# Performance work log

Hardware: AMD Instinct MI355X
Metric: run time of the kernel (lower is better)

The kernel has to match this reference:

```python
import jax, jax.numpy as jnp
import numpy as np

N_HEAD = 16
HEAD_DIM = 64
R_VALUE = 256
EPS_LN = 1e-5


def _orf(x, omega, b):
    # orthogonal random features: sqrt(2/r) * cos(x @ omega.T + b)
    r = b.shape[0]
    return jnp.sqrt(2.0 / r) * jnp.cos(x @ omega.T + b)


def _layernorm(x, gamma, beta):
    m = jnp.mean(x, axis=-1, keepdims=True)
    v = jnp.var(x, axis=-1, keepdims=True)
    return (x - m) / jnp.sqrt(v + EPS_LN) * gamma + beta


def setup_inputs() -> dict:
    key = jax.random.key(0)
    ks = jax.random.split(key, 12)
    B, L = 4, 2048
    dm = N_HEAD * HEAD_DIM  # 1024
    inp = {}
    inp["pre_query"] = jax.random.normal(ks[0], (B, L, dm), jnp.float32)
    inp["pre_key"] = jax.random.normal(ks[1], (B, L, dm), jnp.float32)
    inp["pre_value"] = jax.random.normal(ks[2], (B, L, dm), jnp.float32)
    inp["wq"] = jax.random.normal(ks[3], (dm, dm), jnp.float32) * 0.02
    inp["wk"] = jax.random.normal(ks[4], (dm, dm), jnp.float32) * 0.02
    inp["wv"] = jax.random.normal(ks[5], (dm, dm), jnp.float32) * 0.02
    inp["wo"] = jax.random.normal(ks[6], (dm, dm), jnp.float32) * 0.02
    inp["gamma"] = jnp.ones((dm,), jnp.float32)
    inp["beta"] = jnp.zeros((dm,), jnp.float32)
    G = jax.random.normal(ks[7], (R_VALUE, HEAD_DIM), jnp.float32)
    omega, _ = jnp.linalg.qr(G)  # (r, head_dim), orthonormal columns
    inp["omega"] = omega
    inp["b"] = jax.random.uniform(ks[8], (R_VALUE,), jnp.float32) * 2.0 * jnp.pi
    return inp


def reference(pre_query, pre_key, pre_value, wq, wk, wv, wo, gamma, beta, omega, b):
    B, L, dm = pre_query.shape
    H, D = N_HEAD, dm // N_HEAD
    q = (pre_query @ wq.T).reshape(B, L, H, D)
    k = (pre_key @ wk.T).reshape(B, L, H, D)
    v = (pre_value @ wv.T).reshape(B, L, H, D)

    qp = _orf(q, omega, b)  # (B,L,H,R)
    kp = _orf(k, omega, b)  # (B,L,H,R)

    # causal Performer attention as a linear-attention recurrence:
    # S_t = S_{t-1} + k'_t v_t^T ; z_t = z_{t-1} + k'_t
    # out_t = (q'_t . S_t) / clamp(q'_t . z_t)
    R = b.shape[0]
    S0 = jnp.zeros((B, H, R, D), qp.dtype)
    z0 = jnp.zeros((B, H, R), qp.dtype)

    def step(carry, xs):
        S, z = carry
        q_t, k_t, v_t = xs  # (B,H,R),(B,H,R),(B,H,D)
        S = S + k_t[..., :, None] * v_t[..., None, :]
        z = z + k_t
        num = jnp.einsum('bhr,bhrd->bhd', q_t, S)
        den = jnp.clip(jnp.einsum('bhr,bhr->bh', q_t, z), 1e-6, None)
        return (S, z), num / (den[..., None] + 1e-6)

    xs = (qp.transpose(1, 0, 2, 3), kp.transpose(1, 0, 2, 3), v.transpose(1, 0, 2, 3))
    _, out = jax.lax.scan(step, (S0, z0), xs)  # (L,B,H,D)
    out = out.transpose(1, 0, 2, 3).reshape(B, L, dm)

    pre_result = out @ wo.T
    return _layernorm(pre_result + pre_query, gamma, beta)
```

## Files before the change

### kernel.cpp

```cpp
#include <hip/hip_runtime.h>
#include <hip/hip_bf16.h>


typedef float f4 __attribute__((ext_vector_type(4)));
typedef __attribute__((ext_vector_type(8))) short bf16x8;
typedef __attribute__((ext_vector_type(4))) float f32x4;
typedef unsigned short u16x4 __attribute__((ext_vector_type(4)));
typedef unsigned short u16x8 __attribute__((ext_vector_type(8)));

#define B_  4
#define L_  2048
#define H_  16
#define D_  64
#define DM_ 1024
#define R_  256
#define C_  64
#define NC_ (L_ / C_)
#define M_  (B_ * L_)
#define M2_ (M_ * H_)

static __device__ __forceinline__ unsigned short f2bu(float x) {
    __hip_bfloat16 h = __float2bfloat16(x);
    return *(unsigned short*)&h;
}
static __device__ __forceinline__ float bu2f(unsigned short u) {
    union { unsigned int i; float f; } c; c.i = ((unsigned int)u) << 16; return c.f;
}

typedef __attribute__((address_space(3))) void lds_void_t;
typedef __attribute__((address_space(1))) const void gvoid_t;
static __device__ __forceinline__ void gload16(const void* g, void* l) {
    __builtin_amdgcn_global_load_lds((gvoid_t*)g, (lds_void_t*)l, 16, 0, 0);
}

__launch_bounds__(256)
__global__ void cvt_bf16(const float* __restrict__ in, unsigned short* __restrict__ out, int n4) {
    int i = blockIdx.x * 256 + threadIdx.x;
    if (i < n4) {
        f4 v = *(const f4*)&in[(size_t)i * 4];
        ushort4 o;
        o.x = f2bu(v[0]); o.y = f2bu(v[1]); o.z = f2bu(v[2]); o.w = f2bu(v[3]);
        *(ushort4*)&out[(size_t)i * 4] = o;
    }
}

__launch_bounds__(256)
__global__ void cvt_bf16_x3(const float* __restrict__ i0, const float* __restrict__ i1,
                            const float* __restrict__ i2,
                            unsigned short* __restrict__ o0, unsigned short* __restrict__ o1,
                            unsigned short* __restrict__ o2, int n4) {
    const int z = blockIdx.z;
    const float* in = (z == 0) ? i0 : (z == 1) ? i1 : i2;
    unsigned short* out = (z == 0) ? o0 : (z == 1) ? o1 : o2;
    int i = blockIdx.x * 256 + threadIdx.x;
    if (i < n4) {
        f4 v = *(const f4*)&in[(size_t)i * 4];
        ushort4 o;
        o.x = f2bu(v[0]); o.y = f2bu(v[1]); o.z = f2bu(v[2]); o.w = f2bu(v[3]);
        *(ushort4*)&out[(size_t)i * 4] = o;
    }
}

__launch_bounds__(256)
__global__ void cvt_bf16_x4(const float* __restrict__ i0, const float* __restrict__ i1,
                            const float* __restrict__ i2, const float* __restrict__ i3,
                            unsigned short* __restrict__ o0, unsigned short* __restrict__ o1,
                            unsigned short* __restrict__ o2, unsigned short* __restrict__ o3,
                            int n4_abc, int n4_d) {
    const int z = blockIdx.z;
    const float* in = (z == 0) ? i0 : (z == 1) ? i1 : (z == 2) ? i2 : i3;
    unsigned short* out = (z == 0) ? o0 : (z == 1) ? o1 : (z == 2) ? o2 : o3;
    const int n4 = (z == 3) ? n4_d : n4_abc;
    int i = blockIdx.x * 256 + threadIdx.x;
    if (i < n4) {
        f4 v = *(const f4*)&in[(size_t)i * 4];
        ushort4 o;
        o.x = f2bu(v[0]); o.y = f2bu(v[1]); o.z = f2bu(v[2]); o.w = f2bu(v[3]);
        *(ushort4*)&out[(size_t)i * 4] = o;
    }
}

__launch_bounds__(256)
__global__ void gemm_mfma_b3(const unsigned short* __restrict__ A0, const unsigned short* __restrict__ A1,
                             const unsigned short* __restrict__ A2,
                             const unsigned short* __restrict__ B0, const unsigned short* __restrict__ B1,
                             const unsigned short* __restrict__ B2,
                             unsigned short* __restrict__ C0, unsigned short* __restrict__ C1,
                             unsigned short* __restrict__ C2,
                             int M, int N, int K) {
    __shared__ unsigned short Asl[3][128 * 32];
    __shared__ unsigned short Bsl[3][128 * 32];
    const int z = blockIdx.z;
    const unsigned short* A  = (z == 0) ? A0 : (z == 1) ? A1 : A2;
    const unsigned short* Bw = (z == 0) ? B0 : (z == 1) ? B1 : B2;
    unsigned short*       Cb = (z == 0) ? C0 : (z == 1) ? C1 : C2;
    const int t = threadIdx.x;
    const int lane = t & 63, w = t >> 6;
    const int wr = w >> 1, wc = w & 1;
    const int nwg = gridDim.x * gridDim.y;
    const int bid = blockIdx.y * gridDim.x + blockIdx.x;
    const int cpx = nwg >> 3;
    const int swz = (bid & 7) * cpx + (bid >> 3);
    const int row0 = (swz / gridDim.x) * 128, col0 = (swz % gridDim.x) * 128;
    const int sr0 = t >> 2;
    const int ssw = (((t & 3) ^ ((t >> 3) & 3)) * 8);
    const int lg = lane >> 4, lr = lane & 15;
    const int aslot = (lg ^ ((lr >> 1) & 3)) * 8;

#define STAGE_B3(buf, kkk) do { \
        gload16(&A [(size_t)(row0 + sr0)      * K + (kkk) + ssw], &Asl[buf][t * 8]); \
        gload16(&A [(size_t)(row0 + sr0 + 64) * K + (kkk) + ssw], &Asl[buf][(t + 256) * 8]); \
        gload16(&Bw[(size_t)(col0 + sr0)      * K + (kkk) + ssw], &Bsl[buf][t * 8]); \
        gload16(&Bw[(size_t)(col0 + sr0 + 64) * K + (kkk) + ssw], &Bsl[buf][(t + 256) * 8]); \
    } while (0)
#define COMPUTE_B3(buf) do { \
        bf16x8 af[4], bfr[4]; \
        _Pragma("unroll") \
        for (int m = 0; m < 4; ++m) \
            af[m] = *(const bf16x8*)&Asl[buf][(wr * 64 + m * 16 + lr) * 32 + aslot]; \
        _Pragma("unroll") \
        for (int n = 0; n < 4; ++n) \
            bfr[n] = *(const bf16x8*)&Bsl[buf][(wc * 64 + n * 16 + lr) * 32 + aslot]; \
        _Pragma("unroll") \
        for (int m = 0; m < 4; ++m) \
            _Pragma("unroll") \
            for (int n = 0; n < 4; ++n) \
                acc[m][n] = __builtin_amdgcn_mfma_f32_16x16x32_bf16(af[m], bfr[n], acc[m][n], 0, 0, 0); \
    } while (0)

    f32x4 acc[4][4] = {};
    STAGE_B3(0, 0);
    STAGE_B3(1, 32);
    int cur = 0;
    for (int kk = 0; kk + 64 < K; kk += 32) {
        int nx = cur + 2; if (nx >= 3) nx -= 3;
        STAGE_B3(nx, kk + 64);
        asm volatile("s_waitcnt vmcnt(8)" ::: "memory");
        __builtin_amdgcn_sched_barrier(0);
        __builtin_amdgcn_s_barrier();
        COMPUTE_B3(cur);
        __builtin_amdgcn_s_barrier();
        cur = (cur == 2) ? 0 : cur + 1;
    }
    asm volatile("s_waitcnt vmcnt(4)" ::: "memory");
    __builtin_amdgcn_sched_barrier(0);
    __builtin_amdgcn_s_barrier();
    COMPUTE_B3(cur);
    __builtin_amdgcn_s_barrier();
    cur = (cur == 2) ? 0 : cur + 1;
    asm volatile("s_waitcnt vmcnt(0)" ::: "memory");
    __builtin_amdgcn_sched_barrier(0);
    __builtin_amdgcn_s_barrier();
    COMPUTE_B3(cur);
#undef STAGE_B3
#undef COMPUTE_B3
#pragma unroll
    for (int m = 0; m < 4; ++m)
#pragma unroll
        for (int n = 0; n < 4; ++n)
#pragma unroll
            for (int i = 0; i < 4; ++i) {
                int r  = row0 + wr * 64 + m * 16 + lg * 4 + i;
                int cc = col0 + wc * 64 + n * 16 + lr;
                Cb[(size_t)r * N + cc] = f2bu(acc[m][n][i]);
            }
}

__launch_bounds__(256)
__global__ void gemm_out(const unsigned short* __restrict__ A,
                         const unsigned short* __restrict__ Bw,
                         const float* __restrict__ resid,
                         float* __restrict__ Cf,
                         int M, int N, int K) {
    __shared__ unsigned short Asl[3][64 * 32];
    __shared__ unsigned short Bsl[3][128 * 32];
    const int t = threadIdx.x;
    const int lane = t & 63, w = t >> 6;
    const int nwg = gridDim.x * gridDim.y;
    const int bid = blockIdx.y * gridDim.x + blockIdx.x;
    const int cpx = nwg >> 3;
    const int swz = (bid & 7) * cpx + (bid >> 3);
    const int row0 = (swz / gridDim.x) * 64, col0 = (swz % gridDim.x) * 128;
    const int sr0 = t >> 2;
    const int ssw = (((t & 3) ^ ((t >> 3) & 3)) * 8);
    const int lg = lane >> 4, lr = lane & 15;
    const int aslot = (lg ^ ((lr >> 1) & 3)) * 8;

#define STAGE_O(buf, kkk) do { \
        gload16(&A [(size_t)(row0 + sr0)      * K + (kkk) + ssw], &Asl[buf][t * 8]); \
        gload16(&Bw[(size_t)(col0 + sr0)      * K + (kkk) + ssw], &Bsl[buf][t * 8]); \
        gload16(&Bw[(size_t)(col0 + sr0 + 64) * K + (kkk) + ssw], &Bsl[buf][(t + 256) * 8]); \
    } while (0)
#define COMPUTE_O(buf) do { \
        bf16x8 af[4], bfr[2]; \
        _Pragma("unroll") \
        for (int m = 0; m < 4; ++m) \
            af[m] = *(const bf16x8*)&Asl[buf][(m * 16 + lr) * 32 + aslot]; \
        _Pragma("unroll") \
        for (int n = 0; n < 2; ++n) \
            bfr[n] = *(const bf16x8*)&Bsl[buf][(w * 32 + n * 16 + lr) * 32 + aslot]; \
        _Pragma("unroll") \
        for (int m = 0; m < 4; ++m) \
            _Pragma("unroll") \
            for (int n = 0; n < 2; ++n) \
                acc[m][n] = __builtin_amdgcn_mfma_f32_16x16x32_bf16(af[m], bfr[n], acc[m][n], 0, 0, 0); \
    } while (0)

    f32x4 acc[4][2] = {};
    STAGE_O(0, 0);
    STAGE_O(1, 32);
    int cur = 0;
    for (int kk = 0; kk + 64 < K; kk += 32) {
        int nx = cur + 2; if (nx >= 3) nx -= 3;
        STAGE_O(nx, kk + 64);
        asm volatile("s_waitcnt vmcnt(6)" ::: "memory");
        __builtin_amdgcn_sched_barrier(0);
        __builtin_amdgcn_s_barrier();
        COMPUTE_O(cur);
        __builtin_amdgcn_s_barrier();
        cur = (cur == 2) ? 0 : cur + 1;
    }
    asm volatile("s_waitcnt vmcnt(3)" ::: "memory");
    __builtin_amdgcn_sched_barrier(0);
    __builtin_amdgcn_s_barrier();
    COMPUTE_O(cur);
    __builtin_amdgcn_s_barrier();
    cur = (cur == 2) ? 0 : cur + 1;
    asm volatile("s_waitcnt vmcnt(0)" ::: "memory");
    __builtin_amdgcn_sched_barrier(0);
    __builtin_amdgcn_s_barrier();
    COMPUTE_O(cur);
#undef STAGE_O
#undef COMPUTE_O
#pragma unroll
    for (int m = 0; m < 4; ++m)
#pragma unroll
        for (int n = 0; n < 2; ++n)
#pragma unroll
            for (int i = 0; i < 4; ++i) {
                int r  = row0 + m * 16 + lg * 4 + i;
                int cc = col0 + w * 32 + n * 16 + lr;
                size_t off = (size_t)r * N + cc;
                Cf[off] = acc[m][n][i] + resid[off];
            }
}

#define RS_STRIDE 272
__launch_bounds__(256)
__global__ void feat_mfma_b2(const unsigned short* __restrict__ X0, const unsigned short* __restrict__ X1,
                             const unsigned short* __restrict__ om,
                             const float* __restrict__ bvec,
                             unsigned short* __restrict__ O0, unsigned short* __restrict__ O1) {
    __shared__ unsigned short Xs[2 * 64 * 32];
    __shared__ unsigned short Pool[64 * RS_STRIDE];
    const int z = blockIdx.z;
    const unsigned short* X = z ? X1 : X0;
    unsigned short* out = z ? O1 : O0;
    const int t = threadIdx.x;
    const int lane = t & 63, w = t >> 6;
    const int lg = lane >> 4, lr = lane & 15;
    const int m0 = blockIdx.x * 64;
    const int aslot = (lg ^ ((lr >> 1) & 3)) * 8;

#pragma unroll
    for (int i = 0; i < 2; ++i) {
        int cch = i * 256 + t;
        int ks = cch >> 8, row = (cch >> 2) & 63;
        int sub = ((cch & 3) ^ ((cch >> 3) & 3)) * 8;
        gload16(&X[(size_t)(m0 + row) * 64 + ks * 32 + sub], &Xs[cch * 8]);
    }
#pragma unroll
    for (int i = 0; i < 8; ++i) {
        int cch = i * 256 + t;
        int ks = cch >> 10, r = (cch >> 2) & 255;
        int sub = ((cch & 3) ^ ((cch >> 3) & 3)) * 8;
        gload16(&om[(size_t)r * 64 + ks * 32 + sub], &Pool[cch * 8]);
    }
    __syncthreads();

    f32x4 acc[4][4] = {};
#pragma unroll
    for (int ks = 0; ks < 2; ++ks) {
        bf16x8 af[4], bfr[4];
#pragma unroll
        for (int m = 0; m < 4; ++m)
            af[m] = *(const bf16x8*)&Xs[ks * 2048 + (m * 16 + lr) * 32 + aslot];
#pragma unroll
        for (int n = 0; n < 4; ++n)
            bfr[n] = *(const bf16x8*)&Pool[ks * 8192 + (w * 64 + n * 16 + lr) * 32 + aslot];
#pragma unroll
        for (int m = 0; m < 4; ++m)
#pragma unroll
            for (int n = 0; n < 4; ++n)
                acc[m][n] = __builtin_amdgcn_mfma_f32_16x16x32_bf16(af[m], bfr[n], acc[m][n], 0, 0, 0);
    }
    __syncthreads();

    const float scale = 0.08838834764831845f;
#pragma unroll
    for (int n = 0; n < 4; ++n) {
        const int col = w * 64 + n * 16 + lr;
        const float bb = bvec[col];
#pragma unroll
        for (int m = 0; m < 4; ++m)
#pragma unroll
            for (int ii = 0; ii < 4; ++ii)
                Pool[(m * 16 + lg * 4 + ii) * RS_STRIDE + col] = f2bu(scale * __cosf(acc[m][n][ii] + bb));
    }
    __syncthreads();
#pragma unroll
    for (int i = 0; i < 8; ++i) {
        int cch = i * 256 + t;
        int row = cch >> 5, colc = (cch & 31) * 8;
        u16x8 vv = *(const u16x8*)&Pool[row * RS_STRIDE + colc];
        *(u16x8*)&out[(size_t)(m0 + row) * 256 + colc] = vv;
    }
}

__launch_bounds__(256)
__global__ void passA_mfma(const unsigned short* __restrict__ kp, const unsigned short* __restrict__ vb,
                           unsigned short* __restrict__ kvT, float* __restrict__ ksum) {
    __shared__ __align__(16) unsigned short KPt[256][72];
    __shared__ __align__(16) unsigned short Vt[64][72];
    const int c = blockIdx.x, h = blockIdx.y, bz = blockIdx.z;
    const int t = threadIdx.x;
    const int lane = t & 63, w = t >> 6;
    const int lg = lane >> 4, lr = lane & 15;
    const int l0 = c * C_;
    const int bh = bz * H_ + h;

    {
        const int l4 = (t & 15) * 4, rs = (t >> 4) * 16;
        u16x8 row[4][2];
#pragma unroll
        for (int i = 0; i < 4; ++i) {
            const unsigned short* src = &kp[((size_t)(bz * L_ + l0 + l4 + i) * H_ + h) * R_ + rs];
            row[i][0] = *(const u16x8*)src;
            row[i][1] = *(const u16x8*)(src + 8);
        }
#pragma unroll
        for (int q = 0; q < 16; ++q) {
            u16x4 pk = { row[0][q >> 3][q & 7], row[1][q >> 3][q & 7],
                         row[2][q >> 3][q & 7], row[3][q >> 3][q & 7] };
            *(u16x4*)&KPt[rs + q][l4] = pk;
        }
    }
    {
        const int d4 = (t & 15) * 4, ls = (t >> 4) * 4;
        u16x4 x[4];
#pragma unroll
        for (int i = 0; i < 4; ++i)
            x[i] = *(const u16x4*)&vb[(size_t)(bz * L_ + l0 + ls + i) * DM_ + h * 64 + d4];
#pragma unroll
        for (int q = 0; q < 4; ++q) {
            u16x4 pk = { x[0][q], x[1][q], x[2][q], x[3][q] };
            *(u16x4*)&Vt[d4 + q][ls] = pk;
        }
    }
    __syncthreads();

    f32x4 acc[4][4] = {};
#pragma unroll
    for (int ks = 0; ks < 2; ++ks) {
        bf16x8 af[4], bfr[4];
#pragma unroll
        for (int m = 0; m < 4; ++m)
            af[m] = *(const bf16x8*)&KPt[64 * w + 16 * m + lr][ks * 32 + lg * 8];
#pragma unroll
        for (int n = 0; n < 4; ++n)
            bfr[n] = *(const bf16x8*)&Vt[16 * n + lr][ks * 32 + lg * 8];
#pragma unroll
        for (int m = 0; m < 4; ++m)
#pragma unroll
            for (int n = 0; n < 4; ++n)
                acc[m][n] = __builtin_amdgcn_mfma_f32_16x16x32_bf16(af[m], bfr[n], acc[m][n], 0, 0, 0);
    }
    size_t sbase = ((size_t)(bh * NC_ + c)) * 64 * R_;
#pragma unroll
    for (int n = 0; n < 4; ++n)
#pragma unroll
        for (int m = 0; m < 4; ++m) {
            int d = 16 * n + lr;
            int r = 64 * w + 16 * m + lg * 4;
            u16x4 pk = { f2bu(acc[m][n][0]), f2bu(acc[m][n][1]),
                         f2bu(acc[m][n][2]), f2bu(acc[m][n][3]) };
            *(u16x4*)&kvT[sbase + (size_t)d * R_ + r] = pk;
        }
    {
        float s = 0.f;
#pragma unroll
        for (int j = 0; j < 8; ++j) {
            u16x8 vv = *(const u16x8*)&KPt[t][j * 8];
#pragma unroll
            for (int q = 0; q < 8; ++q) s += bu2f(vv[q]);
        }
        ksum[((size_t)(bh * NC_ + c)) * R_ + t] = s;
    }
}

__launch_bounds__(256)
__global__ void passB_chain(unsigned short* __restrict__ kvT, float* __restrict__ ksum) {
    const int bx = blockIdx.x, h = blockIdx.y, bz = blockIdx.z;
    const int t = threadIdx.x;
    const int bh = bz * H_ + h;
    const int idx = bx * 256 + t;
    const int d = idx >> 6;
    const int rg = (idx & 63) * 4;
    size_t base = ((size_t)bh * NC_ * 64 + d) * R_ + rg;
    const size_t cstride = (size_t)64 * R_;
    float run0 = 0.f, run1 = 0.f, run2 = 0.f, run3 = 0.f;
    for (int c = 0; c < NC_; ++c) {
        size_t ix = base + (size_t)c * cstride;
        u16x4 v = *(const u16x4*)&kvT[ix];
        u16x4 o = { f2bu(run0), f2bu(run1), f2bu(run2), f2bu(run3) };
        *(u16x4*)&kvT[ix] = o;
        run0 += bu2f(v[0]); run1 += bu2f(v[1]);
        run2 += bu2f(v[2]); run3 += bu2f(v[3]);
    }
    if (bx == 0) {
        float rz = 0.f;
        for (int c = 0; c < NC_; ++c) {
            size_t ix = ((size_t)bh * NC_ + c) * R_ + t;
            float tmp = ksum[ix];
            ksum[ix] = rz;
            rz += tmp;
        }
    }
}

__launch_bounds__(256)
__global__ void passC_mfma(const unsigned short* __restrict__ qp, const unsigned short* __restrict__ kp,
                           const unsigned short* __restrict__ vb, const unsigned short* __restrict__ kvT,
                           const float* __restrict__ zpref, unsigned short* __restrict__ attnb) {
    __shared__ __align__(16) unsigned short Sl[64 * 256];
    __shared__ __align__(16) unsigned short Vt[80][72];
    __shared__ __align__(16) unsigned short As[64][72];

    const int c = blockIdx.x, h = blockIdx.y, bz = blockIdx.z;
    const int t = threadIdx.x;
    const int lane = t & 63, w = t >> 6;
    const int lg = lane >> 4, lr = lane & 15;
    const int l0 = c * C_;
    const int bh = bz * H_ + h;
    const size_t sbase = ((size_t)(bh * NC_ + c)) * 64 * R_;
    const size_t zbase = ((size_t)(bh * NC_ + c)) * R_;

#pragma unroll
    for (int i = 0; i < 8; ++i) {
        int idx = i * 256 + t;
        int row = idx >> 5, s = idx & 31;
        gload16(&kvT[sbase + (size_t)row * R_ + ((s ^ (row & 7)) << 3)], &Sl[idx * 8]);
    }

    {
        const int d4 = (t & 15) * 4, ls = (t >> 4) * 4;
        u16x4 x[4];
#pragma unroll
        for (int i = 0; i < 4; ++i)
            x[i] = *(const u16x4*)&vb[(size_t)(bz * L_ + l0 + ls + i) * DM_ + h * 64 + d4];
#pragma unroll
        for (int q = 0; q < 4; ++q) {
            u16x4 pk = { x[0][q], x[1][q], x[2][q], x[3][q] };
            *(u16x4*)&Vt[d4 + q][ls] = pk;
        }
    }
    if (t < 16) {
        u16x4 ones = { 0x3F80, 0x3F80, 0x3F80, 0x3F80 };
        *(u16x4*)&Vt[64][t * 4] = ones;
    }

    const size_t qrow = ((size_t)(bz * L_ + l0 + 16 * w + lr) * H_ + h) * R_;
    bf16x8 aq[8];
#pragma unroll
    for (int ks = 0; ks < 8; ++ks) aq[ks] = *(const bf16x8*)&qp[qrow + ks * 32 + lg * 8];

    f32x4 sacc[4] = {};
#pragma unroll
    for (int half = 0; half < 2; ++half) {
        bf16x8 bk[4][4];
#pragma unroll
        for (int k2 = 0; k2 < 4; ++k2)
#pragma unroll
            for (int n = 0; n < 4; ++n)
                bk[k2][n] = *(const bf16x8*)&kp[((size_t)(bz * L_ + l0 + 16 * n + lr) * H_ + h) * R_
                                                + (half * 4 + k2) * 32 + lg * 8];
        __builtin_amdgcn_s_setprio(1);
#pragma unroll
        for (int k2 = 0; k2 < 4; ++k2)
#pragma unroll
            for (int n = 0; n < 4; ++n)
                sacc[n] = __builtin_amdgcn_mfma_f32_16x16x32_bf16(aq[half * 4 + k2], bk[k2][n], sacc[n], 0, 0, 0);
        __builtin_amdgcn_s_setprio(0);
    }
#pragma unroll
    for (int n = 0; n < 4; ++n)
#pragma unroll
        for (int ii = 0; ii < 4; ++ii) {
            int i_loc = 16 * w + lg * 4 + ii;
            int j_loc = 16 * n + lr;
            As[i_loc][j_loc] = (j_loc <= i_loc) ? f2bu(sacc[n][ii]) : (unsigned short)0;
        }

    u16x8 zu[8];
#pragma unroll
    for (int ks = 0; ks < 8; ++ks) {
        f4 z0 = *(const f4*)&zpref[zbase + ks * 32 + lg * 8];
        f4 z1 = *(const f4*)&zpref[zbase + ks * 32 + lg * 8 + 4];
        zu[ks] = u16x8{ f2bu(z0[0]), f2bu(z0[1]), f2bu(z0[2]), f2bu(z0[3]),
                        f2bu(z1[0]), f2bu(z1[1]), f2bu(z1[2]), f2bu(z1[3]) };
    }
    __syncthreads();

    f32x4 oacc[4] = {};
    f32x4 dacc = {};
    __builtin_amdgcn_s_setprio(1);
#pragma unroll
    for (int ks = 0; ks < 8; ++ks) {
#pragma unroll
        for (int n = 0; n < 4; ++n) {
            int row = 16 * n + lr;
            int slot = (ks * 4 + lg) ^ (lr & 7);
            bf16x8 bs = *(const bf16x8*)&Sl[row * 256 + slot * 8];
            oacc[n] = __builtin_amdgcn_mfma_f32_16x16x32_bf16(aq[ks], bs, oacc[n], 0, 0, 0);
        }
        dacc = __builtin_amdgcn_mfma_f32_16x16x32_bf16(aq[ks], *(bf16x8*)&zu[ks], dacc, 0, 0, 0);
    }

    f32x4 racc = {};
#pragma unroll
    for (int ks = 0; ks < 2; ++ks) {
        bf16x8 aa = *(const bf16x8*)&As[16 * w + lr][ks * 32 + lg * 8];
#pragma unroll
        for (int n = 0; n < 4; ++n) {
            bf16x8 bv = *(const bf16x8*)&Vt[16 * n + lr][ks * 32 + lg * 8];
            oacc[n] = __builtin_amdgcn_mfma_f32_16x16x32_bf16(aa, bv, oacc[n], 0, 0, 0);
        }
        bf16x8 b4 = *(const bf16x8*)&Vt[64 + lr][ks * 32 + lg * 8];
        racc = __builtin_amdgcn_mfma_f32_16x16x32_bf16(aa, b4, racc, 0, 0, 0);
    }
    __builtin_amdgcn_s_setprio(0);

#pragma unroll
    for (int ii = 0; ii < 4; ++ii) {
        float rs_ = __shfl(racc[ii], lane & 48, 64);
        float den = rs_ + dacc[ii];
        float inv = 1.f / (fmaxf(den, 1e-6f) + 1e-6f);
#pragma unroll
        for (int n = 0; n < 4; ++n)
            attnb[(size_t)(bz * L_ + l0 + 16 * w + lg * 4 + ii) * DM_ + h * 64 + 16 * n + lr] =
                f2bu(oacc[n][ii] * inv);
    }
}

__launch_bounds__(256)
__global__ void ln_kernel(float* __restrict__ io, const float* __restrict__ gamma,
                          const float* __restrict__ beta) {
    __shared__ float wsum[4], wsum2[4];
    const int row = blockIdx.x;
    const int t = threadIdx.x;
    f4 x = *(const f4*)&io[(size_t)row * DM_ + t * 4];
    float s  = x[0] + x[1] + x[2] + x[3];
    float s2 = x[0]*x[0] + x[1]*x[1] + x[2]*x[2] + x[3]*x[3];
#pragma unroll
    for (int o = 32; o > 0; o >>= 1) {
        s  += __shfl_down(s, o);
        s2 += __shfl_down(s2, o);
    }
    if ((t & 63) == 0) { wsum[t >> 6] = s; wsum2[t >> 6] = s2; }
    __syncthreads();
    s  = wsum[0]  + wsum[1]  + wsum[2]  + wsum[3];
    s2 = wsum2[0] + wsum2[1] + wsum2[2] + wsum2[3];
    const float m = s * (1.f / DM_);
    const float var = s2 * (1.f / DM_) - m * m;
    const float rstd = rsqrtf(var + 1e-5f);
    f4 g  = *(const f4*)&gamma[t * 4];
    f4 bb = *(const f4*)&beta[t * 4];
    f4 o = (x - m) * rstd * g + bb;
    *(f4*)&io[(size_t)row * DM_ + t * 4] = o;
}

extern "C" void kernel_launch(void* const* d_in, const int* in_sizes, int n_in,
                              void* d_out, int out_size, void* d_ws, size_t ws_size,
                              hipStream_t stream) {
    const float* pre_q = (const float*)d_in[0];
    const float* pre_k = (const float*)d_in[1];
    const float* pre_v = (const float*)d_in[2];
    const float* wq    = (const float*)d_in[3];
    const float* wk    = (const float*)d_in[4];
    const float* wv    = (const float*)d_in[5];
    const float* wo    = (const float*)d_in[6];
    const float* gamma = (const float*)d_in[7];
    const float* beta  = (const float*)d_in[8];
    const float* omega = (const float*)d_in[9];
    const float* bvec  = (const float*)d_in[10];

    const size_t NEED = 226ull << 20;
    if (ws_size < NEED) return;

    char* w = (char*)d_ws;
    unsigned short* qp    = (unsigned short*)(w);
    unsigned short* kp    = (unsigned short*)(w + (64ull << 20));
    unsigned short* kvT   = (unsigned short*)(w + (128ull << 20));
    unsigned short* vb    = (unsigned short*)(w + (192ull << 20));
    unsigned short* attnb = (unsigned short*)(w + (208ull << 20));
    float*          ksum  = (float*)(w + (224ull << 20));
    unsigned short* aq    = (unsigned short*)(w);
    unsigned short* ak    = (unsigned short*)(w + (16ull << 20));
    unsigned short* av    = (unsigned short*)(w + (32ull << 20));
    unsigned short* wq_bf = (unsigned short*)(w + (48ull << 20));
    unsigned short* wk_bf = (unsigned short*)(w + (50ull << 20));
    unsigned short* wv_bf = (unsigned short*)(w + (52ull << 20));
    unsigned short* qx    = (unsigned short*)(w + (128ull << 20));
    unsigned short* kx    = (unsigned short*)(w + (144ull << 20));
    unsigned short* om_bf = (unsigned short*)(w + (208ull << 20));
    unsigned short* wo_bf = (unsigned short*)(w + (64ull << 20));
    float*          outb  = (float*)d_out;

    const int n4_big = M_ * DM_ / 4;
    const int n4_w   = DM_ * DM_ / 4;
    const int n4_om  = R_ * D_ / 4;
    dim3 gg3(DM_ / 128, M_ / 128, 3);
    dim3 ggo(DM_ / 128, M_ / 64);

    cvt_bf16_x3<<<dim3((n4_big + 255) / 256, 1, 3), 256, 0, stream>>>(
        pre_q, pre_k, pre_v, aq, ak, av, n4_big);
    cvt_bf16_x4<<<dim3((n4_w + 255) / 256, 1, 4), 256, 0, stream>>>(
        wq, wk, wv, omega, wq_bf, wk_bf, wv_bf, om_bf, n4_w, n4_om);

    gemm_mfma_b3<<<gg3, 256, 0, stream>>>(aq, ak, av, wq_bf, wk_bf, wv_bf,
                                          qx, kx, vb, M_, DM_, DM_);
    feat_mfma_b2<<<dim3(M2_ / 64, 1, 2), 256, 0, stream>>>(qx, kx, om_bf, bvec, qp, kp);

    passA_mfma<<<dim3(NC_, H_, B_), 256, 0, stream>>>(kp, vb, kvT, ksum);
    passB_chain<<<dim3(16, H_, B_), 256, 0, stream>>>(kvT, ksum);
    passC_mfma<<<dim3(NC_, H_, B_), 256, 0, stream>>>(qp, kp, vb, kvT, ksum, attnb);

    cvt_bf16<<<(n4_w + 255) / 256, 256, 0, stream>>>(wo, wo_bf, n4_w);
    gemm_out<<<ggo, 256, 0, stream>>>(attnb, wo_bf, pre_q, outb, M_, DM_, DM_);
    ln_kernel<<<M_, 256, 0, stream>>>(outb, gamma, beta);
}
```

Measured before the change: 289.4 us.

## Fuse fp32-to-bf16 activation conversion into the QKV projection GEMM

Removes the separate pass that converts the three fp32 input activations to bf16. The QKV GEMM now loads fp32 A tiles into registers, converts them, and writes bf16 into LDS, with register prefetch two tiles ahead and a double-buffered LDS pipeline instead of triple buffering. This saves a full write and re-read of three 16 MB bf16 intermediates plus a kernel launch. In exchange each GEMM fetches twice as many bytes for A, converts in the main loop, and raises wave priority around the MFMA block.

```diff
diff --git a/kernel.cpp b/kernel.cpp
--- a/kernel.cpp
+++ b/kernel.cpp
@@ -35,23 +35,6 @@
 
 __launch_bounds__(256)
 __global__ void cvt_bf16(const float* __restrict__ in, unsigned short* __restrict__ out, int n4) {
-    int i = blockIdx.x * 256 + threadIdx.x;
-    if (i < n4) {
-        f4 v = *(const f4*)&in[(size_t)i * 4];
-        ushort4 o;
-        o.x = f2bu(v[0]); o.y = f2bu(v[1]); o.z = f2bu(v[2]); o.w = f2bu(v[3]);
-        *(ushort4*)&out[(size_t)i * 4] = o;
-    }
-}
-
-__launch_bounds__(256)
-__global__ void cvt_bf16_x3(const float* __restrict__ i0, const float* __restrict__ i1,
-                            const float* __restrict__ i2,
-                            unsigned short* __restrict__ o0, unsigned short* __restrict__ o1,
-                            unsigned short* __restrict__ o2, int n4) {
-    const int z = blockIdx.z;
-    const float* in = (z == 0) ? i0 : (z == 1) ? i1 : i2;
-    unsigned short* out = (z == 0) ? o0 : (z == 1) ? o1 : o2;
     int i = blockIdx.x * 256 + threadIdx.x;
     if (i < n4) {
         f4 v = *(const f4*)&in[(size_t)i * 4];
@@ -81,17 +64,17 @@
 }
 
 __launch_bounds__(256)
-__global__ void gemm_mfma_b3(const unsigned short* __restrict__ A0, const unsigned short* __restrict__ A1,
-                             const unsigned short* __restrict__ A2,
-                             const unsigned short* __restrict__ B0, const unsigned short* __restrict__ B1,
-                             const unsigned short* __restrict__ B2,
-                             unsigned short* __restrict__ C0, unsigned short* __restrict__ C1,
-                             unsigned short* __restrict__ C2,
-                             int M, int N, int K) {
-    __shared__ unsigned short Asl[3][128 * 32];
-    __shared__ unsigned short Bsl[3][128 * 32];
+__global__ void gemm_qkv(const float* __restrict__ A0, const float* __restrict__ A1,
+                         const float* __restrict__ A2,
+                         const unsigned short* __restrict__ B0, const unsigned short* __restrict__ B1,
+                         const unsigned short* __restrict__ B2,
+                         unsigned short* __restrict__ C0, unsigned short* __restrict__ C1,
+                         unsigned short* __restrict__ C2,
+                         int M, int N, int K) {
+    __shared__ unsigned short Asl[2][128 * 32];
+    __shared__ unsigned short Bsl[2][128 * 32];
     const int z = blockIdx.z;
-    const unsigned short* A  = (z == 0) ? A0 : (z == 1) ? A1 : A2;
+    const float* A = (z == 0) ? A0 : (z == 1) ? A1 : A2;
     const unsigned short* Bw = (z == 0) ? B0 : (z == 1) ? B1 : B2;
     unsigned short*       Cb = (z == 0) ? C0 : (z == 1) ? C1 : C2;
     const int t = threadIdx.x;
@@ -107,13 +90,42 @@
     const int lg = lane >> 4, lr = lane & 15;
     const int aslot = (lg ^ ((lr >> 1) & 3)) * 8;
 
-#define STAGE_B3(buf, kkk) do { \
-        gload16(&A [(size_t)(row0 + sr0)      * K + (kkk) + ssw], &Asl[buf][t * 8]); \
-        gload16(&A [(size_t)(row0 + sr0 + 64) * K + (kkk) + ssw], &Asl[buf][(t + 256) * 8]); \
+    f4 s0a, s0b, s0c, s0d;
+    f4 s1a, s1b, s1c, s1d;
+
+#define LOADA0(kkk) do { \
+        s0a = *(const f4*)&A[(size_t)(row0 + sr0)      * K + (kkk) + ssw]; \
+        s0b = *(const f4*)&A[(size_t)(row0 + sr0)      * K + (kkk) + ssw + 4]; \
+        s0c = *(const f4*)&A[(size_t)(row0 + sr0 + 64) * K + (kkk) + ssw]; \
+        s0d = *(const f4*)&A[(size_t)(row0 + sr0 + 64) * K + (kkk) + ssw + 4]; \
+    } while (0)
+#define LOADA1(kkk) do { \
+        s1a = *(const f4*)&A[(size_t)(row0 + sr0)      * K + (kkk) + ssw]; \
+        s1b = *(const f4*)&A[(size_t)(row0 + sr0)      * K + (kkk) + ssw + 4]; \
+        s1c = *(const f4*)&A[(size_t)(row0 + sr0 + 64) * K + (kkk) + ssw]; \
+        s1d = *(const f4*)&A[(size_t)(row0 + sr0 + 64) * K + (kkk) + ssw + 4]; \
+    } while (0)
+#define WRITEA0(buf) do { \
+        u16x8 w0 = { f2bu(s0a[0]), f2bu(s0a[1]), f2bu(s0a[2]), f2bu(s0a[3]), \
+                     f2bu(s0b[0]), f2bu(s0b[1]), f2bu(s0b[2]), f2bu(s0b[3]) }; \
+        u16x8 w1 = { f2bu(s0c[0]), f2bu(s0c[1]), f2bu(s0c[2]), f2bu(s0c[3]), \
+                     f2bu(s0d[0]), f2bu(s0d[1]), f2bu(s0d[2]), f2bu(s0d[3]) }; \
+        *(u16x8*)&Asl[buf][t * 8] = w0; \
+        *(u16x8*)&Asl[buf][(t + 256) * 8] = w1; \
+    } while (0)
+#define WRITEA1(buf) do { \
+        u16x8 w0 = { f2bu(s1a[0]), f2bu(s1a[1]), f2bu(s1a[2]), f2bu(s1a[3]), \
+                     f2bu(s1b[0]), f2bu(s1b[1]), f2bu(s1b[2]), f2bu(s1b[3]) }; \
+        u16x8 w1 = { f2bu(s1c[0]), f2bu(s1c[1]), f2bu(s1c[2]), f2bu(s1c[3]), \
+                     f2bu(s1d[0]), f2bu(s1d[1]), f2bu(s1d[2]), f2bu(s1d[3]) }; \
+        *(u16x8*)&Asl[buf][t * 8] = w0; \
+        *(u16x8*)&Asl[buf][(t + 256) * 8] = w1; \
+    } while (0)
+#define STAGEB(buf, kkk) do { \
         gload16(&Bw[(size_t)(col0 + sr0)      * K + (kkk) + ssw], &Bsl[buf][t * 8]); \
         gload16(&Bw[(size_t)(col0 + sr0 + 64) * K + (kkk) + ssw], &Bsl[buf][(t + 256) * 8]); \
     } while (0)
-#define COMPUTE_B3(buf) do { \
+#define COMPUTE(buf) do { \
         bf16x8 af[4], bfr[4]; \
         _Pragma("unroll") \
         for (int m = 0; m < 4; ++m) \
@@ -121,39 +133,62 @@
         _Pragma("unroll") \
         for (int n = 0; n < 4; ++n) \
             bfr[n] = *(const bf16x8*)&Bsl[buf][(wc * 64 + n * 16 + lr) * 32 + aslot]; \
+        __builtin_amdgcn_s_setprio(1); \
         _Pragma("unroll") \
         for (int m = 0; m < 4; ++m) \
             _Pragma("unroll") \
             for (int n = 0; n < 4; ++n) \
                 acc[m][n] = __builtin_amdgcn_mfma_f32_16x16x32_bf16(af[m], bfr[n], acc[m][n], 0, 0, 0); \
+        __builtin_amdgcn_s_setprio(0); \
     } while (0)
 
     f32x4 acc[4][4] = {};
-    STAGE_B3(0, 0);
-    STAGE_B3(1, 32);
-    int cur = 0;
-    for (int kk = 0; kk + 64 < K; kk += 32) {
-        int nx = cur + 2; if (nx >= 3) nx -= 3;
-        STAGE_B3(nx, kk + 64);
-        asm volatile("s_waitcnt vmcnt(8)" ::: "memory");
-        __builtin_amdgcn_sched_barrier(0);
-        __builtin_amdgcn_s_barrier();
-        COMPUTE_B3(cur);
-        __builtin_amdgcn_s_barrier();
-        cur = (cur == 2) ? 0 : cur + 1;
-    }
-    asm volatile("s_waitcnt vmcnt(4)" ::: "memory");
+    const int NT = K >> 5;
+    STAGEB(0, 0);
+    LOADA0(0);
+    LOADA1(32);
+    WRITEA0(0);
+    asm volatile("s_waitcnt lgkmcnt(0)" ::: "memory");
     __builtin_amdgcn_sched_barrier(0);
     __builtin_amdgcn_s_barrier();
-    COMPUTE_B3(cur);
-    __builtin_amdgcn_s_barrier();
-    cur = (cur == 2) ? 0 : cur + 1;
-    asm volatile("s_waitcnt vmcnt(0)" ::: "memory");
-    __builtin_amdgcn_sched_barrier(0);
-    __builtin_amdgcn_s_barrier();
-    COMPUTE_B3(cur);
-#undef STAGE_B3
-#undef COMPUTE_B3
+
+    for (int T = 0; T < NT; T += 2) {
+        {
+            const int hasN = 1;
+            const int has2 = (T + 2 < NT);
+            STAGEB(1, (T + 1) * 32);
+            if (has2) LOADA0((T + 2) * 32);
+            WRITEA1(1);
+            COMPUTE(0);
+            if (has2) { asm volatile("s_waitcnt vmcnt(4)" ::: "memory"); }
+            else      { asm volatile("s_waitcnt vmcnt(0)" ::: "memory"); }
+            __builtin_amdgcn_sched_barrier(0);
+            asm volatile("s_waitcnt lgkmcnt(0)" ::: "memory");
+            __builtin_amdgcn_s_barrier();
+            (void)hasN;
+        }
+        {
+            const int has2 = (T + 2 < NT);
+            const int has3 = (T + 3 < NT);
+            if (has2) STAGEB(0, (T + 2) * 32);
+            if (has3) LOADA1((T + 3) * 32);
+            if (has2) WRITEA0(0);
+            COMPUTE(1);
+            if (has2) {
+                if (has3) { asm volatile("s_waitcnt vmcnt(4)" ::: "memory"); }
+                else      { asm volatile("s_waitcnt vmcnt(0)" ::: "memory"); }
+                __builtin_amdgcn_sched_barrier(0);
+                asm volatile("s_waitcnt lgkmcnt(0)" ::: "memory");
+                __builtin_amdgcn_s_barrier();
+            }
+        }
+    }
+#undef LOADA0
+#undef LOADA1
+#undef WRITEA0
+#undef WRITEA1
+#undef STAGEB
+#undef COMPUTE
 #pragma unroll
     for (int m = 0; m < 4; ++m)
 #pragma unroll
@@ -604,9 +639,6 @@
     unsigned short* vb    = (unsigned short*)(w + (192ull << 20));
     unsigned short* attnb = (unsigned short*)(w + (208ull << 20));
     float*          ksum  = (float*)(w + (224ull << 20));
-    unsigned short* aq    = (unsigned short*)(w);
-    unsigned short* ak    = (unsigned short*)(w + (16ull << 20));
-    unsigned short* av    = (unsigned short*)(w + (32ull << 20));
     unsigned short* wq_bf = (unsigned short*)(w + (48ull << 20));
     unsigned short* wk_bf = (unsigned short*)(w + (50ull << 20));
     unsigned short* wv_bf = (unsigned short*)(w + (52ull << 20));
@@ -616,19 +648,16 @@
     unsigned short* wo_bf = (unsigned short*)(w + (64ull << 20));
     float*          outb  = (float*)d_out;
 
-    const int n4_big = M_ * DM_ / 4;
     const int n4_w   = DM_ * DM_ / 4;
     const int n4_om  = R_ * D_ / 4;
     dim3 gg3(DM_ / 128, M_ / 128, 3);
     dim3 ggo(DM_ / 128, M_ / 64);
 
-    cvt_bf16_x3<<<dim3((n4_big + 255) / 256, 1, 3), 256, 0, stream>>>(
-        pre_q, pre_k, pre_v, aq, ak, av, n4_big);
     cvt_bf16_x4<<<dim3((n4_w + 255) / 256, 1, 4), 256, 0, stream>>>(
         wq, wk, wv, omega, wq_bf, wk_bf, wv_bf, om_bf, n4_w, n4_om);
 
-    gemm_mfma_b3<<<gg3, 256, 0, stream>>>(aq, ak, av, wq_bf, wk_bf, wv_bf,
-                                          qx, kx, vb, M_, DM_, DM_);
+    gemm_qkv<<<gg3, 256, 0, stream>>>(pre_q, pre_k, pre_v, wq_bf, wk_bf, wv_bf,
+                                      qx, kx, vb, M_, DM_, DM_);
     feat_mfma_b2<<<dim3(M2_ / 64, 1, 2), 256, 0, stream>>>(qx, kx, om_bf, bvec, qp, kp);
 
     passA_mfma<<<dim3(NC_, H_, B_), 256, 0, stream>>>(kp, vb, kvT, ksum);
```

After: 327.0 us. 1.13x slower.
